# Optimization experiments

Measured on AMD Instinct MI355X. Metric: run time of the kernel, lower is better.

## Reference

```python
import jax, jax.numpy as jnp
import numpy as np


def setup_inputs() -> dict:
    key = jax.random.key(0)
    ks = jax.random.split(key, 6)
    B, N, F, H, E = 2, 50000, 64, 32, 800000
    x = jax.random.normal(ks[0], (B, N, F), dtype=jnp.float32)
    edge_index = jax.random.randint(ks[1], (2, E), 0, N, dtype=jnp.int64)
    h_cur = jax.random.normal(ks[2], (B, N, H), dtype=jnp.float32)
    c_cur = jax.random.normal(ks[3], (B, N, H), dtype=jnp.float32)
    W = jax.random.normal(ks[4], (F + H, 4 * H), dtype=jnp.float32) * (1.0 / np.sqrt(F + H))
    b = jax.random.normal(ks[5], (4 * H,), dtype=jnp.float32) * 0.01
    return {"x": x, "edge_index": edge_index, "h_cur": h_cur, "c_cur": c_cur, "W": W, "b": b}


def reference(x, edge_index, h_cur, c_cur, W, b):
    B, N, _ = x.shape
    H = h_cur.shape[-1]

    # --- GCNConv on concatenated [x, h] ---
    combined = jnp.concatenate([x, h_cur], axis=-1)          # [B, N, F+H]
    xw = jnp.einsum('bnf,fg->bng', combined, W)              # [B, N, 4H]

    # add self-loops
    loop = jnp.arange(N, dtype=edge_index.dtype)
    src = jnp.concatenate([edge_index[0], loop])             # [E+N]
    dst = jnp.concatenate([edge_index[1], loop])             # [E+N]

    # symmetric degree normalization: deg over target index (PyG gcn_norm)
    deg = jnp.zeros((N,), dtype=xw.dtype).at[dst].add(1.0)
    dinv = jnp.where(deg > 0, jax.lax.rsqrt(deg), 0.0)
    norm = dinv[src] * dinv[dst]                             # [E+N]

    # gather-scale-scatter aggregation
    msgs = xw[:, src, :] * norm[None, :, None]               # [B, E+N, 4H]
    agg = jnp.zeros((B, N, 4 * H), dtype=xw.dtype).at[:, dst, :].add(msgs)
    conv = agg + b                                           # [B, N, 4H]

    # --- LSTM gating ---
    cc_i, cc_f, cc_o, cc_g = jnp.split(conv, 4, axis=-1)
    i = jax.nn.sigmoid(cc_i)
    f = jax.nn.sigmoid(cc_f)
    o = jax.nn.sigmoid(cc_o)
    g = jnp.tanh(cc_g)
    c_next = f * c_cur + i * g
    h_next = o * jnp.tanh(c_next)
    return h_next, c_next
```

## Files before the change

### kernel.cpp

```cpp
#include <hip/hip_runtime.h>
#include <hip/hip_bf16.h>

constexpr int H_DIM = 32;
constexpr int KPAD  = 104;
constexpr int CAP   = 64;
constexpr int CHK   = 64;
constexpr int EPB   = 2048;

typedef __attribute__((ext_vector_type(8))) short bf16x8;
typedef __attribute__((ext_vector_type(4))) float f32x4;

static __device__ __forceinline__ unsigned short f2bf_bits(float v) {
    __hip_bfloat16 b = __float2bfloat16(v);
    return *reinterpret_cast<unsigned short*>(&b);
}
static __device__ __forceinline__ unsigned pack2(float a, float b) {
    return (unsigned)f2bf_bits(a) | ((unsigned)f2bf_bits(b) << 16);
}
static __device__ __forceinline__ float lo_f(unsigned u) { return __uint_as_float(u << 16); }
static __device__ __forceinline__ float hi_f(unsigned u) { return __uint_as_float(u & 0xffff0000u); }

static __device__ __forceinline__ void fma4p(const uint4 u, float d, float* a)
{
    a[0] = fmaf(lo_f(u.x), d, a[0]);
    a[4] = fmaf(hi_f(u.x), d, a[4]);
    a[1] = fmaf(lo_f(u.y), d, a[1]);
    a[5] = fmaf(hi_f(u.y), d, a[5]);
    a[2] = fmaf(lo_f(u.z), d, a[2]);
    a[6] = fmaf(hi_f(u.z), d, a[6]);
    a[3] = fmaf(lo_f(u.w), d, a[3]);
    a[7] = fmaf(hi_f(u.w), d, a[7]);
}

__global__ __launch_bounds__(256)
void part_convert_kernel(const float* __restrict__ x,
                         const float* __restrict__ h,
                         const int* __restrict__ ei,
                         unsigned* __restrict__ part_buf,
                         unsigned char* __restrict__ hcnt,
                         unsigned* __restrict__ z,
                         int N, int E, int NB)
{
    const int bi = blockIdx.x;
    const int t  = threadIdx.x;
    if (bi < NB) {
        __shared__ unsigned loff[256];
        loff[t] = 0u;
        __syncthreads();
        const int e0 = bi * EPB + t;
        #pragma unroll
        for (int j = 0; j < 8; ++j) {
            int e = e0 + 256 * j;
            if (e < E) {
                int src = ei[e];
                int dst = ei[E + e];
                int p   = dst >> 8;
                unsigned pos = atomicAdd(&loff[p], 1u);
                if (pos < CHK)
                    part_buf[((long)p * NB + bi) * CHK + pos] =
                        (unsigned)src | ((unsigned)(dst & 255) << 16);
            }
        }
        __syncthreads();
        hcnt[bi * 256 + t] = (unsigned char)min(loff[t], (unsigned)CHK);
        return;
    }

    long idx = (long)(bi - NB) * 256 + t;
    if (idx >= (long)N * 24) return;
    int n  = (int)(idx / 24);
    int ku = (int)(idx - (long)n * 24);
    int f0 = 4 * ku;
    float4 a, b;
    if (f0 < 64) {
        a = *reinterpret_cast<const float4*>(x + (long)n * 64 + f0);
        b = *reinterpret_cast<const float4*>(x + ((long)N + n) * 64 + f0);
    } else {
        a = *reinterpret_cast<const float4*>(h + (long)n * 32 + (f0 - 64));
        b = *reinterpret_cast<const float4*>(h + ((long)N + n) * 32 + (f0 - 64));
    }
    uint4 o;
    o.x = pack2(a.x, b.x);
    o.y = pack2(a.y, b.y);
    o.z = pack2(a.z, b.z);
    o.w = pack2(a.w, b.w);
    *reinterpret_cast<uint4*>(z + idx * 4) = o;
}

__global__ __launch_bounds__(256)
void bucket_prep_kernel(const unsigned* __restrict__ part_buf,
                        const unsigned char* __restrict__ hcnt,
                        const float* __restrict__ W,
                        unsigned short* __restrict__ Wt,
                        unsigned* __restrict__ cnt,
                        unsigned short* __restrict__ bucket,
                        int N, int NB, int NPART)
{
    const int t = threadIdx.x;
    if ((int)blockIdx.x >= NPART) {
        int gt = ((int)blockIdx.x - NPART) * 256 + t;
        if (gt < 96 * 128) {
            int k = gt >> 7;
            int n = gt & 127;
            Wt[n * 96 + k] = f2bf_bits(W[gt]);
        }
        return;
    }

    __shared__ unsigned lcnt[256];
    __shared__ __align__(16) unsigned short lbuck[256 * CAP];
    const int p = blockIdx.x;
    lcnt[t] = 0u;
    __syncthreads();

    for (int c = t; c < NB; c += 256) {
        int cc = (int)hcnt[c * 256 + p];
        const unsigned* __restrict__ pb = part_buf + ((long)p * NB + c) * CHK;
        for (int jj = 0; jj < cc; jj += 4) {
            uint4 u4 = *reinterpret_cast<const uint4*>(pb + jj);
            unsigned uu[4] = {u4.x, u4.y, u4.z, u4.w};
            #pragma unroll
            for (int q2 = 0; q2 < 4; ++q2) {
                if (jj + q2 < cc) {
                    unsigned u = uu[q2];
                    int dl = (int)((u >> 16) & 0xFFu);
                    unsigned pos = atomicAdd(&lcnt[dl], 1u);
                    if (pos < CAP) lbuck[dl * CAP + pos] = (unsigned short)(u & 0xFFFFu);
                }
            }
        }
    }
    __syncthreads();

    int n = p * 256 + t;
    if (n < N) cnt[n] = lcnt[t];
    #pragma unroll
    for (int j = 0; j < 8; ++j) {
        int idx = t + 256 * j;
        int row = idx >> 3, c = idx & 7;
        int nn = p * 256 + row;
        if (nn < N)
            *reinterpret_cast<uint4*>(bucket + (long)nn * CAP + 8 * c) =
                *reinterpret_cast<const uint4*>(&lbuck[row * CAP + 8 * c]);
    }
}

__global__ __launch_bounds__(256)
void gather_gemm_kernel(const unsigned* __restrict__ cnt,
                        const unsigned short* __restrict__ bucket,
                        const unsigned* __restrict__ z,
                        const unsigned short* __restrict__ Wt,
                        const float* __restrict__ bias,
                        const float* __restrict__ c_cur,
                        float* __restrict__ out,
                        int N)
{
    __shared__ __align__(16) unsigned short As[64 * KPAD];
    const int t    = threadIdx.x;
    const int n0   = blockIdx.x * 32;
    const int wv   = t >> 6;
    const int lane = t & 63;
    const int g    = lane >> 5;
    const int w    = lane & 31;
    const unsigned* __restrict__ zw = z + 4 * w;

    for (int s = 0; s < 8; ++s) {
        const int n    = n0 + wv * 8 + s;
        const bool live = (n < N);
        const int nn   = live ? n : 0;
        const int dn   = live ? min((int)cnt[nn], CAP) : 0;
        const unsigned short* __restrict__ brow = bucket + (long)nn * CAP;

        float acc[8];
        #pragma unroll
        for (int j = 0; j < 8; ++j) acc[j] = 0.f;

        for (int base = 0; base < dn; base += 64) {
            int cnt64 = min(64, dn - base);
            int   s_reg = 0;
            float d_reg = 0.f;
            if (lane < cnt64) {
                s_reg = (int)brow[base + lane];
                d_reg = rsqrtf((float)cnt[s_reg] + 1.f);
            }
            for (int i = 0; i < cnt64; i += 16) {
                int ss[8]; float dd[8]; uint4 u[8];
                #pragma unroll
                for (int j = 0; j < 8; ++j) {
                    int ij = i + 2 * j + g;
                    ss[j] = __shfl(s_reg, ij);
                    dd[j] = __shfl(d_reg, ij);
                    if (ij >= cnt64) dd[j] = 0.f;
                }
                #pragma unroll
                for (int j = 0; j < 8; ++j) {
                    int ij = i + 2 * j + g;
                    u[j] = make_uint4(0u, 0u, 0u, 0u);
                    if (w < 24 && ij < cnt64)
                        u[j] = *reinterpret_cast<const uint4*>(zw + (long)ss[j] * 96);
                }
                #pragma unroll
                for (int j = 0; j < 8; ++j) fma4p(u[j], dd[j], acc);
            }
        }

        #pragma unroll
        for (int j = 0; j < 8; ++j) acc[j] += __shfl_xor(acc[j], 32);

        if (live && g == 0 && w < 24) {
            float di  = rsqrtf((float)cnt[nn] + 1.f);
            float di2 = di * di;
            uint4 us = *reinterpret_cast<const uint4*>(zw + (long)nn * 96);
            float l0 = fmaf(di, acc[0], di2 * lo_f(us.x));
            float l1 = fmaf(di, acc[1], di2 * lo_f(us.y));
            float l2 = fmaf(di, acc[2], di2 * lo_f(us.z));
            float l3 = fmaf(di, acc[3], di2 * lo_f(us.w));
            float h0 = fmaf(di, acc[4], di2 * hi_f(us.x));
            float h1 = fmaf(di, acc[5], di2 * hi_f(us.y));
            float h2 = fmaf(di, acc[6], di2 * hi_f(us.z));
            float h3 = fmaf(di, acc[7], di2 * hi_f(us.w));
            int r0 = wv * 8 + s;
            *reinterpret_cast<uint2*>(&As[r0 * KPAD + 4 * w]) =
                make_uint2(pack2(l0, l1), pack2(l2, l3));
            *reinterpret_cast<uint2*>(&As[(32 + r0) * KPAD + 4 * w]) =
                make_uint2(pack2(h0, h1), pack2(h2, h3));
        }
    }
    __syncthreads();

    const int m = lane & 15;
    const int q = lane >> 4;

    f32x4 acc[8] = {};
    #pragma unroll
    for (int k0 = 0; k0 < 96; k0 += 32) {
        bf16x8 a = *reinterpret_cast<const bf16x8*>(&As[(wv * 16 + m) * KPAD + k0 + q * 8]);
        #pragma unroll
        for (int nt = 0; nt < 8; ++nt) {
            bf16x8 b = *reinterpret_cast<const bf16x8*>(&Wt[(nt * 16 + m) * 96 + k0 + q * 8]);
            acc[nt] = __builtin_amdgcn_mfma_f32_16x16x32_bf16(a, b, acc[nt], 0, 0, 0);
        }
    }

    const float bi0 = bias[m],       bi1 = bias[16 + m];
    const float bf0 = bias[32 + m],  bf1 = bias[48 + m];
    const float bo0 = bias[64 + m],  bo1 = bias[80 + m];
    const float bg0 = bias[96 + m],  bg1 = bias[112 + m];
    const long  co  = (long)2 * N * H_DIM;

    #pragma unroll
    for (int r = 0; r < 4; ++r) {
        int rr = wv * 16 + q * 4 + r;
        int b  = rr >> 5;
        int i  = rr & 31;
        int n  = n0 + i;
        if (n < N) {
            long base = ((long)b * N + n) * H_DIM;
            float c0 = c_cur[base + m];
            float c1 = c_cur[base + 16 + m];
            float ig0 = 1.f / (1.f + __expf(-(acc[0][r] + bi0)));
            float ig1 = 1.f / (1.f + __expf(-(acc[1][r] + bi1)));
            float fg0 = 1.f / (1.f + __expf(-(acc[2][r] + bf0)));
            float fg1 = 1.f / (1.f + __expf(-(acc[3][r] + bf1)));
            float og0 = 1.f / (1.f + __expf(-(acc[4][r] + bo0)));
            float og1 = 1.f / (1.f + __expf(-(acc[5][r] + bo1)));
            float gg0 = tanhf(acc[6][r] + bg0);
            float gg1 = tanhf(acc[7][r] + bg1);
            float cn0 = fmaf(fg0, c0, ig0 * gg0);
            float cn1 = fmaf(fg1, c1, ig1 * gg1);
            out[base + m]           = og0 * tanhf(cn0);
            out[base + 16 + m]      = og1 * tanhf(cn1);
            out[co + base + m]      = cn0;
            out[co + base + 16 + m] = cn1;
        }
    }
}

extern "C" void kernel_launch(void* const* d_in, const int* in_sizes, int n_in,
                              void* d_out, int out_size, void* d_ws, size_t ws_size,
                              hipStream_t stream)
{
    const float* x    = (const float*)d_in[0];
    const int*   ei   = (const int*)d_in[1];
    const float* h    = (const float*)d_in[2];
    const float* c    = (const float*)d_in[3];
    const float* W    = (const float*)d_in[4];
    const float* bias = (const float*)d_in[5];

    const int  E  = in_sizes[1] / 2;
    const long BN = (long)in_sizes[2] / H_DIM;
    const int  N  = (int)(BN / 2);
    const int  NP = (N + 255) >> 8;
    const int  NB = (E + EPB - 1) / EPB;

    char* ws = (char*)d_ws;
    unsigned* z = (unsigned*)ws;
    size_t off = (size_t)N * 96 * sizeof(unsigned);
    unsigned* cnt = (unsigned*)(ws + off);   off += (size_t)N * sizeof(unsigned);
    unsigned short* bucket = (unsigned short*)(ws + off); off += (size_t)N * CAP * sizeof(unsigned short);
    unsigned short* Wt = (unsigned short*)(ws + off);     off += 96 * 128 * sizeof(unsigned short);
    off = (off + 255) & ~(size_t)255;
    unsigned* part_buf = (unsigned*)(ws + off); off += (size_t)NP * NB * CHK * sizeof(unsigned);
    unsigned char* hcnt = (unsigned char*)(ws + off); off += (size_t)NB * 256;

    int convGrid = (int)(((long)N * 24 + 255) / 256);
    part_convert_kernel<<<NB + convGrid, 256, 0, stream>>>(
        x, h, ei, part_buf, hcnt, z, N, E, NB);

    bucket_prep_kernel<<<NP + 48, 256, 0, stream>>>(
        part_buf, hcnt, W, Wt, cnt, bucket, N, NB, NP);

    int mGrid = (N + 31) / 32;
    gather_gemm_kernel<<<mGrid, 256, 0, stream>>>(
        cnt, bucket, z, Wt, bias, c, (float*)d_out, N);
}
```

Baseline: 190.8 us.

## Shrink gather-GEMM blocks to four nodes and split MFMA columns across waves

Each block now handles 4 nodes instead of 32: one wave per node does the neighbor gather, then the small 8-row A tile is multiplied with each wave computing two of the eight 16-column output tiles. Results are staged in shared memory so the LSTM gating runs with one thread per (row, hidden) element, giving coalesced c_cur loads and output stores. The change also moves gather address math to 32-bit offsets. The goal is more blocks for better latency hiding and less serial per-wave work on the gather loop. The cost is that half of each MFMA tile's rows are wasted, the launch grid is eight times larger, and an extra barrier is added.

```diff
diff --git a/kernel.cpp b/kernel.cpp
--- a/kernel.cpp
+++ b/kernel.cpp
@@ -155,17 +155,18 @@
                         float* __restrict__ out,
                         int N)
 {
-    __shared__ __align__(16) unsigned short As[64 * KPAD];
+    __shared__ __align__(16) unsigned short As[16 * KPAD];
+    __shared__ float ccs[8][128];
     const int t    = threadIdx.x;
-    const int n0   = blockIdx.x * 32;
+    const int n0   = blockIdx.x * 4;
     const int wv   = t >> 6;
     const int lane = t & 63;
     const int g    = lane >> 5;
     const int w    = lane & 31;
     const unsigned* __restrict__ zw = z + 4 * w;
 
-    for (int s = 0; s < 8; ++s) {
-        const int n    = n0 + wv * 8 + s;
+    {
+        const int n    = n0 + wv;
         const bool live = (n < N);
         const int nn   = live ? n : 0;
         const int dn   = live ? min((int)cnt[nn], CAP) : 0;
@@ -184,11 +185,11 @@
                 d_reg = rsqrtf((float)cnt[s_reg] + 1.f);
             }
             for (int i = 0; i < cnt64; i += 16) {
-                int ss[8]; float dd[8]; uint4 u[8];
+                unsigned so[8]; float dd[8]; uint4 u[8];
                 #pragma unroll
                 for (int j = 0; j < 8; ++j) {
                     int ij = i + 2 * j + g;
-                    ss[j] = __shfl(s_reg, ij);
+                    so[j] = (unsigned)__shfl(s_reg, ij) * 96u;
                     dd[j] = __shfl(d_reg, ij);
                     if (ij >= cnt64) dd[j] = 0.f;
                 }
@@ -197,7 +198,7 @@
                     int ij = i + 2 * j + g;
                     u[j] = make_uint4(0u, 0u, 0u, 0u);
                     if (w < 24 && ij < cnt64)
-                        u[j] = *reinterpret_cast<const uint4*>(zw + (long)ss[j] * 96);
+                        u[j] = *reinterpret_cast<const uint4*>(zw + so[j]);
                 }
                 #pragma unroll
                 for (int j = 0; j < 8; ++j) fma4p(u[j], dd[j], acc);
@@ -210,7 +211,7 @@
         if (live && g == 0 && w < 24) {
             float di  = rsqrtf((float)cnt[nn] + 1.f);
             float di2 = di * di;
-            uint4 us = *reinterpret_cast<const uint4*>(zw + (long)nn * 96);
+            uint4 us = *reinterpret_cast<const uint4*>(zw + (unsigned)nn * 96u);
             float l0 = fmaf(di, acc[0], di2 * lo_f(us.x));
             float l1 = fmaf(di, acc[1], di2 * lo_f(us.y));
             float l2 = fmaf(di, acc[2], di2 * lo_f(us.z));
@@ -219,10 +220,9 @@
             float h1 = fmaf(di, acc[5], di2 * hi_f(us.y));
             float h2 = fmaf(di, acc[6], di2 * hi_f(us.z));
             float h3 = fmaf(di, acc[7], di2 * hi_f(us.w));
-            int r0 = wv * 8 + s;
-            *reinterpret_cast<uint2*>(&As[r0 * KPAD + 4 * w]) =
+            *reinterpret_cast<uint2*>(&As[wv * KPAD + 4 * w]) =
                 make_uint2(pack2(l0, l1), pack2(l2, l3));
-            *reinterpret_cast<uint2*>(&As[(32 + r0) * KPAD + 4 * w]) =
+            *reinterpret_cast<uint2*>(&As[(4 + wv) * KPAD + 4 * w]) =
                 make_uint2(pack2(h0, h1), pack2(h2, h3));
         }
     }
@@ -231,48 +231,47 @@
     const int m = lane & 15;
     const int q = lane >> 4;
 
-    f32x4 acc[8] = {};
+    f32x4 a2[2] = {};
     #pragma unroll
     for (int k0 = 0; k0 < 96; k0 += 32) {
-        bf16x8 a = *reinterpret_cast<const bf16x8*>(&As[(wv * 16 + m) * KPAD + k0 + q * 8]);
-        #pragma unroll
-        for (int nt = 0; nt < 8; ++nt) {
-            bf16x8 b = *reinterpret_cast<const bf16x8*>(&Wt[(nt * 16 + m) * 96 + k0 + q * 8]);
-            acc[nt] = __builtin_amdgcn_mfma_f32_16x16x32_bf16(a, b, acc[nt], 0, 0, 0);
-        }
-    }
-
-    const float bi0 = bias[m],       bi1 = bias[16 + m];
-    const float bf0 = bias[32 + m],  bf1 = bias[48 + m];
-    const float bo0 = bias[64 + m],  bo1 = bias[80 + m];
-    const float bg0 = bias[96 + m],  bg1 = bias[112 + m];
-    const long  co  = (long)2 * N * H_DIM;
-
-    #pragma unroll
-    for (int r = 0; r < 4; ++r) {
-        int rr = wv * 16 + q * 4 + r;
-        int b  = rr >> 5;
-        int i  = rr & 31;
-        int n  = n0 + i;
-        if (n < N) {
-            long base = ((long)b * N + n) * H_DIM;
-            float c0 = c_cur[base + m];
-            float c1 = c_cur[base + 16 + m];
-            float ig0 = 1.f / (1.f + __expf(-(acc[0][r] + bi0)));
-            float ig1 = 1.f / (1.f + __expf(-(acc[1][r] + bi1)));
-            float fg0 = 1.f / (1.f + __expf(-(acc[2][r] + bf0)));
-            float fg1 = 1.f / (1.f + __expf(-(acc[3][r] + bf1)));
-            float og0 = 1.f / (1.f + __expf(-(acc[4][r] + bo0)));
-            float og1 = 1.f / (1.f + __expf(-(acc[5][r] + bo1)));
-            float gg0 = tanhf(acc[6][r] + bg0);
-            float gg1 = tanhf(acc[7][r] + bg1);
-            float cn0 = fmaf(fg0, c0, ig0 * gg0);
-            float cn1 = fmaf(fg1, c1, ig1 * gg1);
-            out[base + m]           = og0 * tanhf(cn0);
-            out[base + 16 + m]      = og1 * tanhf(cn1);
-            out[co + base + m]      = cn0;
-            out[co + base + 16 + m] = cn1;
-        }
+        bf16x8 a = *reinterpret_cast<const bf16x8*>(&As[m * KPAD + k0 + q * 8]);
+        #pragma unroll
+        for (int ntl = 0; ntl < 2; ++ntl) {
+            int ct = 2 * wv + ntl;
+            bf16x8 b = *reinterpret_cast<const bf16x8*>(&Wt[(ct * 16 + m) * 96 + k0 + q * 8]);
+            a2[ntl] = __builtin_amdgcn_mfma_f32_16x16x32_bf16(a, b, a2[ntl], 0, 0, 0);
+        }
+    }
+
+    if (lane < 32) {
+        #pragma unroll
+        for (int ntl = 0; ntl < 2; ++ntl) {
+            int col = (2 * wv + ntl) * 16 + m;
+            #pragma unroll
+            for (int r = 0; r < 4; ++r)
+                ccs[q * 4 + r][col] = a2[ntl][r];
+        }
+    }
+    __syncthreads();
+
+    const int row = t >> 5;
+    const int l   = t & 31;
+    const int b   = row >> 2;
+    const int ni  = n0 + (row & 3);
+    if (ni < N) {
+        float cc0 = ccs[row][l]      + bias[l];
+        float cc1 = ccs[row][32 + l] + bias[32 + l];
+        float cc2 = ccs[row][64 + l] + bias[64 + l];
+        float cc3 = ccs[row][96 + l] + bias[96 + l];
+        float ig = 1.f / (1.f + __expf(-cc0));
+        float fg = 1.f / (1.f + __expf(-cc1));
+        float og = 1.f / (1.f + __expf(-cc2));
+        float gg = tanhf(cc3);
+        long basei = ((long)b * N + ni) * H_DIM + l;
+        float c  = c_cur[basei];
+        float cn = fmaf(fg, c, ig * gg);
+        out[basei]                       = og * tanhf(cn);
+        out[(long)2 * N * H_DIM + basei] = cn;
     }
 }
 
@@ -310,7 +309,7 @@
     bucket_prep_kernel<<<NP + 48, 256, 0, stream>>>(
         part_buf, hcnt, W, Wt, cnt, bucket, N, NB, NP);
 
-    int mGrid = (N + 31) / 32;
+    int mGrid = (N + 3) / 4;
     gather_gemm_kernel<<<mGrid, 256, 0, stream>>>(
         cnt, bucket, z, Wt, bias, c, (float*)d_out, N);
 }
```

New measurement: 187.9 us, median of 3. No clear change (-1.5%).

## Split fused gather+GEMM into separate gather and GEMM/gates kernels

Applied to the files above, without the earlier changes.

Splits the fused gather-then-MFMA kernel into two. The new gather kernel uses one wavefront per node across the whole grid, and every one of the 32 lanes loads a uint3 instead of 24 lanes loading a uint4. It writes the normalized aggregate to a new workspace buffer. A second kernel reloads that buffer into LDS and runs the MFMA GEMM with the LSTM gating. The aim is more parallelism and fully used lanes in the latency-bound gather, at the cost of an extra global round trip of N*96 words and one more kernel launch.

```diff
diff --git a/kernel.cpp b/kernel.cpp
--- a/kernel.cpp
+++ b/kernel.cpp
@@ -20,16 +20,14 @@
 static __device__ __forceinline__ float lo_f(unsigned u) { return __uint_as_float(u << 16); }
 static __device__ __forceinline__ float hi_f(unsigned u) { return __uint_as_float(u & 0xffff0000u); }
 
-static __device__ __forceinline__ void fma4p(const uint4 u, float d, float* a)
+static __device__ __forceinline__ void fma3p(const uint3 u, float d, float* a)
 {
     a[0] = fmaf(lo_f(u.x), d, a[0]);
-    a[4] = fmaf(hi_f(u.x), d, a[4]);
+    a[3] = fmaf(hi_f(u.x), d, a[3]);
     a[1] = fmaf(lo_f(u.y), d, a[1]);
-    a[5] = fmaf(hi_f(u.y), d, a[5]);
+    a[4] = fmaf(hi_f(u.y), d, a[4]);
     a[2] = fmaf(lo_f(u.z), d, a[2]);
-    a[6] = fmaf(hi_f(u.z), d, a[6]);
-    a[3] = fmaf(lo_f(u.w), d, a[3]);
-    a[7] = fmaf(hi_f(u.w), d, a[7]);
+    a[5] = fmaf(hi_f(u.z), d, a[5]);
 }
 
 __global__ __launch_bounds__(256)
@@ -146,90 +144,104 @@
 }
 
 __global__ __launch_bounds__(256)
-void gather_gemm_kernel(const unsigned* __restrict__ cnt,
-                        const unsigned short* __restrict__ bucket,
-                        const unsigned* __restrict__ z,
-                        const unsigned short* __restrict__ Wt,
-                        const float* __restrict__ bias,
-                        const float* __restrict__ c_cur,
-                        float* __restrict__ out,
-                        int N)
+void gather_kernel(const unsigned* __restrict__ cnt,
+                   const unsigned short* __restrict__ bucket,
+                   const unsigned* __restrict__ z,
+                   unsigned* __restrict__ aggz, int N)
+{
+    const int wid  = (int)(((long)blockIdx.x * 256 + threadIdx.x) >> 6);
+    const int lane = threadIdx.x & 63;
+    const int g    = lane >> 5;
+    const int w    = lane & 31;
+    const bool live = (wid < N);
+    const int n = live ? wid : 0;
+
+    const int dn = live ? min((int)cnt[n], CAP) : 0;
+    const unsigned short* __restrict__ brow = bucket + (long)n * CAP;
+    const unsigned* __restrict__ zw = z + 3 * w;
+
+    float acc[6];
+    #pragma unroll
+    for (int j = 0; j < 6; ++j) acc[j] = 0.f;
+
+    for (int base = 0; base < dn; base += 64) {
+        int cnt64 = min(64, dn - base);
+        int   s_reg = 0;
+        float d_reg = 0.f;
+        if (lane < cnt64) {
+            s_reg = (int)brow[base + lane];
+            d_reg = rsqrtf((float)cnt[s_reg] + 1.f);
+        }
+        for (int i = 0; i < cnt64; i += 16) {
+            unsigned so[8]; float dd[8]; uint3 u[8];
+            #pragma unroll
+            for (int j = 0; j < 8; ++j) {
+                int ij = i + 2 * j + g;
+                so[j] = (unsigned)__shfl(s_reg, ij) * 96u;
+                dd[j] = __shfl(d_reg, ij);
+                if (ij >= cnt64) dd[j] = 0.f;
+            }
+            #pragma unroll
+            for (int j = 0; j < 8; ++j) {
+                int ij = i + 2 * j + g;
+                u[j] = make_uint3(0u, 0u, 0u);
+                if (ij < cnt64)
+                    u[j] = *reinterpret_cast<const uint3*>(zw + so[j]);
+            }
+            #pragma unroll
+            for (int j = 0; j < 8; ++j) fma3p(u[j], dd[j], acc);
+        }
+    }
+
+    #pragma unroll
+    for (int j = 0; j < 6; ++j) acc[j] += __shfl_xor(acc[j], 32);
+
+    if (live && g == 0) {
+        float di  = rsqrtf((float)cnt[n] + 1.f);
+        float di2 = di * di;
+        uint3 us = *reinterpret_cast<const uint3*>(zw + (unsigned)n * 96u);
+        uint3 o;
+        o.x = pack2(fmaf(di, acc[0], di2 * lo_f(us.x)), fmaf(di, acc[3], di2 * hi_f(us.x)));
+        o.y = pack2(fmaf(di, acc[1], di2 * lo_f(us.y)), fmaf(di, acc[4], di2 * hi_f(us.y)));
+        o.z = pack2(fmaf(di, acc[2], di2 * lo_f(us.z)), fmaf(di, acc[5], di2 * hi_f(us.z)));
+        *reinterpret_cast<uint3*>(aggz + (unsigned)n * 96u + 3 * w) = o;
+    }
+}
+
+__global__ __launch_bounds__(256)
+void gemm_gates_kernel(const unsigned* __restrict__ aggz,
+                       const unsigned short* __restrict__ Wt,
+                       const float* __restrict__ bias,
+                       const float* __restrict__ c_cur,
+                       float* __restrict__ out,
+                       int N)
 {
     __shared__ __align__(16) unsigned short As[64 * KPAD];
-    const int t    = threadIdx.x;
-    const int n0   = blockIdx.x * 32;
+    const int t  = threadIdx.x;
+    const int n0 = blockIdx.x * 32;
+
+    #pragma unroll
+    for (int j = 0; j < 3; ++j) {
+        int idx = t + 256 * j;
+        int i   = idx / 24;
+        int ku  = idx - 24 * i;
+        int n   = n0 + i;
+        uint4 u = make_uint4(0,0,0,0);
+        if (n < N) u = *reinterpret_cast<const uint4*>(aggz + (long)n * 96 + 4 * ku);
+        ushort4 lo, hi;
+        lo.x = (unsigned short)u.x;  hi.x = (unsigned short)(u.x >> 16);
+        lo.y = (unsigned short)u.y;  hi.y = (unsigned short)(u.y >> 16);
+        lo.z = (unsigned short)u.z;  hi.z = (unsigned short)(u.z >> 16);
+        lo.w = (unsigned short)u.w;  hi.w = (unsigned short)(u.w >> 16);
+        *reinterpret_cast<ushort4*>(&As[i * KPAD + 4 * ku])        = lo;
+        *reinterpret_cast<ushort4*>(&As[(32 + i) * KPAD + 4 * ku]) = hi;
+    }
+    __syncthreads();
+
     const int wv   = t >> 6;
     const int lane = t & 63;
-    const int g    = lane >> 5;
-    const int w    = lane & 31;
-    const unsigned* __restrict__ zw = z + 4 * w;
-
-    for (int s = 0; s < 8; ++s) {
-        const int n    = n0 + wv * 8 + s;
-        const bool live = (n < N);
-        const int nn   = live ? n : 0;
-        const int dn   = live ? min((int)cnt[nn], CAP) : 0;
-        const unsigned short* __restrict__ brow = bucket + (long)nn * CAP;
-
-        float acc[8];
-        #pragma unroll
-        for (int j = 0; j < 8; ++j) acc[j] = 0.f;
-
-        for (int base = 0; base < dn; base += 64) {
-            int cnt64 = min(64, dn - base);
-            int   s_reg = 0;
-            float d_reg = 0.f;
-            if (lane < cnt64) {
-                s_reg = (int)brow[base + lane];
-                d_reg = rsqrtf((float)cnt[s_reg] + 1.f);
-            }
-            for (int i = 0; i < cnt64; i += 16) {
-                int ss[8]; float dd[8]; uint4 u[8];
-                #pragma unroll
-                for (int j = 0; j < 8; ++j) {
-                    int ij = i + 2 * j + g;
-                    ss[j] = __shfl(s_reg, ij);
-                    dd[j] = __shfl(d_reg, ij);
-                    if (ij >= cnt64) dd[j] = 0.f;
-                }
-                #pragma unroll
-                for (int j = 0; j < 8; ++j) {
-                    int ij = i + 2 * j + g;
-                    u[j] = make_uint4(0u, 0u, 0u, 0u);
-                    if (w < 24 && ij < cnt64)
-                        u[j] = *reinterpret_cast<const uint4*>(zw + (long)ss[j] * 96);
-                }
-                #pragma unroll
-                for (int j = 0; j < 8; ++j) fma4p(u[j], dd[j], acc);
-            }
-        }
-
-        #pragma unroll
-        for (int j = 0; j < 8; ++j) acc[j] += __shfl_xor(acc[j], 32);
-
-        if (live && g == 0 && w < 24) {
-            float di  = rsqrtf((float)cnt[nn] + 1.f);
-            float di2 = di * di;
-            uint4 us = *reinterpret_cast<const uint4*>(zw + (long)nn * 96);
-            float l0 = fmaf(di, acc[0], di2 * lo_f(us.x));
-            float l1 = fmaf(di, acc[1], di2 * lo_f(us.y));
-            float l2 = fmaf(di, acc[2], di2 * lo_f(us.z));
-            float l3 = fmaf(di, acc[3], di2 * lo_f(us.w));
-            float h0 = fmaf(di, acc[4], di2 * hi_f(us.x));
-            float h1 = fmaf(di, acc[5], di2 * hi_f(us.y));
-            float h2 = fmaf(di, acc[6], di2 * hi_f(us.z));
-            float h3 = fmaf(di, acc[7], di2 * hi_f(us.w));
-            int r0 = wv * 8 + s;
-            *reinterpret_cast<uint2*>(&As[r0 * KPAD + 4 * w]) =
-                make_uint2(pack2(l0, l1), pack2(l2, l3));
-            *reinterpret_cast<uint2*>(&As[(32 + r0) * KPAD + 4 * w]) =
-                make_uint2(pack2(h0, h1), pack2(h2, h3));
-        }
-    }
-    __syncthreads();
-
-    const int m = lane & 15;
-    const int q = lane >> 4;
+    const int m    = lane & 15;
+    const int q    = lane >> 4;
 
     f32x4 acc[8] = {};
     #pragma unroll
@@ -296,7 +308,8 @@
     char* ws = (char*)d_ws;
     unsigned* z = (unsigned*)ws;
     size_t off = (size_t)N * 96 * sizeof(unsigned);
-    unsigned* cnt = (unsigned*)(ws + off);   off += (size_t)N * sizeof(unsigned);
+    unsigned* aggz = (unsigned*)(ws + off);  off += (size_t)N * 96 * sizeof(unsigned);
+    unsigned* cnt  = (unsigned*)(ws + off);  off += (size_t)N * sizeof(unsigned);
     unsigned short* bucket = (unsigned short*)(ws + off); off += (size_t)N * CAP * sizeof(unsigned short);
     unsigned short* Wt = (unsigned short*)(ws + off);     off += 96 * 128 * sizeof(unsigned short);
     off = (off + 255) & ~(size_t)255;
@@ -310,7 +323,9 @@
     bucket_prep_kernel<<<NP + 48, 256, 0, stream>>>(
         part_buf, hcnt, W, Wt, cnt, bucket, N, NB, NP);
 
+    int gGrid = (int)(((long)N * 64 + 255) / 256);
+    gather_kernel<<<gGrid, 256, 0, stream>>>(cnt, bucket, z, aggz, N);
+
     int mGrid = (N + 31) / 32;
-    gather_gemm_kernel<<<mGrid, 256, 0, stream>>>(
-        cnt, bucket, z, Wt, bias, c, (float*)d_out, N);
-}
+    gemm_gates_kernel<<<mGrid, 256, 0, stream>>>(aggz, Wt, bias, c, (float*)d_out, N);
+}
```

New measurement: 189.1 us. About the same (-0.9%).
